# Kernel optimization log

Measured on AMD Instinct MI355X. Metric: run time of the kernel, lower is better.

## Reference

```python
import jax, jax.numpy as jnp
import numpy as np

B, N, E, H = 2, 2048, 768, 12
D = E // H          # head_dim = 64
G = 16              # gate_dim
LN_EPS = 1e-5


def setup_inputs() -> dict:
    key = jax.random.key(0)
    ks = jax.random.split(key, 8)
    s = E ** -0.5
    x = jax.random.normal(ks[0], (B, N, E), jnp.float32)
    # per-head negative decay slopes (ALiBi/TNL-style)
    log_slope = -(2.0 ** (-8.0 * (jnp.arange(H, dtype=jnp.float32) + 1.0) / H))
    Wq = jax.random.normal(ks[1], (E, E), jnp.float32) * s
    Wk = jax.random.normal(ks[2], (E, E), jnp.float32) * s
    Wv = jax.random.normal(ks[3], (E, E), jnp.float32) * s
    Wo = jax.random.normal(ks[4], (E, E), jnp.float32) * s
    Wg1 = jax.random.normal(ks[5], (E, G), jnp.float32) * s
    Wg2 = jax.random.normal(ks[6], (G, E), jnp.float32) * (G ** -0.5)
    ln_w = jnp.ones((E,), jnp.float32)
    ln_b = jnp.zeros((E,), jnp.float32)
    return {"x": x, "log_slope": log_slope, "Wq": Wq, "Wk": Wk, "Wv": Wv,
            "Wo": Wo, "Wg1": Wg1, "Wg2": Wg2, "ln_w": ln_w, "ln_b": ln_b}


def _layernorm(x, w, b):
    mu = jnp.mean(x, axis=-1, keepdims=True)
    var = jnp.mean(jnp.square(x - mu), axis=-1, keepdims=True)
    return (x - mu) * jax.lax.rsqrt(var + LN_EPS) * w + b


def reference(x, log_slope, Wq, Wk, Wv, Wo, Wg1, Wg2, ln_w, ln_b):
    b, n, e = x.shape
    h = log_slope.shape[0]
    d = e // h
    silu = jax.nn.silu
    q = silu(x @ Wq).reshape(b, n, h, d).transpose(0, 2, 1, 3)  # b h n d
    k = silu(x @ Wk).reshape(b, n, h, d).transpose(0, 2, 1, 3)
    v = silu(x @ Wv).reshape(b, n, h, d).transpose(0, 2, 1, 3)

    # exp-decay causal mask: exp(log_slope * (i - j)) for i >= j, else 0
    idx = jnp.arange(n, dtype=jnp.float32)
    diff = idx[:, None] - idx[None, :]                    # n x m
    keep = diff >= 0
    decay = jnp.where(keep,
                      jnp.exp(log_slope[:, None, None] * jnp.maximum(diff, 0.0)),
                      0.0)                                # h n m

    energy = jnp.einsum('bhnd,bhmd->bhnm', q, k) * decay  # b h n m
    out = jnp.einsum('bhnm,bhmd->bhnd', energy, v)        # b h n d
    out = out.transpose(0, 2, 1, 3).reshape(b, n, e)

    gate = jax.nn.sigmoid((x @ Wg1) @ Wg2)                # low-rank output gate
    out = out * gate
    out = out @ Wo
    out = _layernorm(out, ln_w, ln_b)                     # norm_pos='post'
    return out
```

## Files before the change

### kernel.cpp

```cpp
#include <hip/hip_runtime.h>
#include <stdint.h>

#define BB 2
#define NN 2048
#define EE 768
#define HH 12
#define DD 64
#define GG 16

typedef unsigned short u16;
typedef unsigned int u32;
typedef __attribute__((ext_vector_type(8))) short short8;
typedef __attribute__((ext_vector_type(4))) float f32x4;
typedef __attribute__((ext_vector_type(4))) unsigned short u16x4;

__device__ __forceinline__ u16 f2bf(float f) {
  union { float f; u32 u; } a; a.f = f;
  u32 r = a.u + 0x7FFFu + ((a.u >> 16) & 1u);
  return (u16)(r >> 16);
}
__device__ __forceinline__ float bf2f(short s) {
  union { u32 u; float f; } a; a.u = ((u32)(u16)s) << 16; return a.f;
}

__device__ __forceinline__ float silu_f(float v) { return v / (1.f + __expf(-v)); }

__device__ __forceinline__ void gload16(const u16* g, char* l) {
  __builtin_amdgcn_global_load_lds(
      (const __attribute__((address_space(1))) void*)(g),
      (__attribute__((address_space(3))) void*)(l), 16, 0, 0);
}

template<int ROWS>
__device__ __forceinline__ void stage_tile(const u16* __restrict__ gb, int ld, int row0, int col0,
                                           char* lds, int tid) {
  int wid = tid >> 6;
#pragma unroll
  for (int it = 0; it < ROWS / 32; ++it) {
    int c = it * 256 + tid;
    int r = c >> 3;
    int g = (c & 7) ^ (r & 7);
    gload16(gb + (size_t)(row0 + r) * ld + col0 + g * 8,
            lds + (it * 256 + wid * 64) * 16);
  }
}

__device__ __forceinline__ void stage_S(const u16* __restrict__ base, char* lds, int tid, int plane) {
  int wid = tid >> 6;
#pragma unroll
  for (int it = 0; it < 2; ++it) {
    int c = it * 256 + tid;
    int r = c >> 3;
    int g = (c & 7) ^ (r & 7);
    gload16(base + (r >> 4) * 2048 + plane * 1024 + (r & 15) * 64 + g * 8,
            lds + (it * 256 + wid * 64) * 16);
  }
}

__device__ __forceinline__ short8 read_frag(const char* lds, int row, int gk) {
  return *(const short8*)(lds + (((row << 3) | (gk ^ (row & 7))) << 4));
}

__device__ __forceinline__ short8 scale_frag(short8 f, float sc) {
  short8 o;
#pragma unroll
  for (int i = 0; i < 8; ++i) o[i] = (short)f2bf(bf2f(f[i]) * sc);
  return o;
}

__global__ __launch_bounds__(256) void xconv_kernel(const float* __restrict__ x, u16* __restrict__ xb) {
  int i = blockIdx.x * 256 + threadIdx.x;
  float4 v = ((const float4*)x)[i];
  u16x4 o;
  o.x = f2bf(v.x); o.y = f2bf(v.y); o.z = f2bf(v.z); o.w = f2bf(v.w);
  ((u16x4*)xb)[i] = o;
}

__global__ __launch_bounds__(256) void wconv_kernel(const float* __restrict__ Wq, const float* __restrict__ Wk,
    const float* __restrict__ Wv, const float* __restrict__ Wo,
    u16* __restrict__ Wqt, u16* __restrict__ Wkt, u16* __restrict__ Wvt, u16* __restrict__ Wot) {
  const float* src; u16* dst;
  int z = blockIdx.z;
  if (z == 0)      { src = Wq; dst = Wqt; }
  else if (z == 1) { src = Wk; dst = Wkt; }
  else if (z == 2) { src = Wv; dst = Wvt; }
  else             { src = Wo; dst = Wot; }
  __shared__ float tb[64][65];
  int k0 = blockIdx.x * 64, n0 = blockIdx.y * 64;
  int tid = threadIdx.x;
#pragma unroll
  for (int i = 0; i < 16; ++i) {
    int idx = i * 256 + tid;
    int r = idx >> 6, c = idx & 63;
    tb[r][c] = src[(size_t)(k0 + r) * EE + n0 + c];
  }
  __syncthreads();
#pragma unroll
  for (int i = 0; i < 16; ++i) {
    int idx = i * 256 + tid;
    int rn = idx >> 6, ck = idx & 63;
    dst[(size_t)(n0 + rn) * EE + k0 + ck] = f2bf(tb[ck][rn]);
  }
}

__global__ __launch_bounds__(256) void tg_kernel(const float* __restrict__ x, const float* __restrict__ Wg1,
                                                 float* __restrict__ tg) {
  int tid = threadIdx.x, lane = tid & 63, wid = tid >> 6;
  int m = blockIdx.x * 4 + wid;
  int col = lane & 15, sl = lane >> 4;
  const float* xr = x + (size_t)m * EE + sl * 192;
  float acc = 0.f;
#pragma unroll 4
  for (int i = 0; i < 48; ++i) {
    float4 xv = ((const float4*)xr)[i];
    int kk = sl * 192 + i * 4;
    acc += xv.x * Wg1[(kk + 0) * GG + col];
    acc += xv.y * Wg1[(kk + 1) * GG + col];
    acc += xv.z * Wg1[(kk + 2) * GG + col];
    acc += xv.w * Wg1[(kk + 3) * GG + col];
  }
  acc += __shfl_down(acc, 32);
  acc += __shfl_down(acc, 16);
  if (lane < 16) tg[(size_t)m * GG + col] = acc;
}

__global__ __launch_bounds__(256) void qkv_gemm(const u16* __restrict__ xb,
    const u16* __restrict__ Wqt, const u16* __restrict__ Wkt, const u16* __restrict__ Wvt,
    u16* __restrict__ qp, u16* __restrict__ kp, u16* __restrict__ vtp) {
  __shared__ __attribute__((aligned(16))) char As[16384];
  __shared__ __attribute__((aligned(16))) char Zs[16384];
  int tid = threadIdx.x, lane = tid & 63, wid = tid >> 6;
  int m0 = blockIdx.x * 128, n0 = blockIdx.y * 128, w = blockIdx.z;
  const u16* Zt = (w == 0) ? Wqt : (w == 1) ? Wkt : Wvt;
  int wm = wid >> 1, wn = wid & 1;
  f32x4 acc[4][4] = {};
  for (int kt = 0; kt < EE / 64; ++kt) {
    __syncthreads();
    stage_tile<128>(xb, EE, m0, kt * 64, As, tid);
    stage_tile<128>(Zt, EE, n0, kt * 64, Zs, tid);
    __syncthreads();
    short8 af[2][4], bfr[2][4];
#pragma unroll
    for (int ds = 0; ds < 2; ++ds) {
      int gk = ds * 4 + (lane >> 4);
#pragma unroll
      for (int i = 0; i < 4; ++i) {
        af[ds][i]  = read_frag(As, wm * 64 + i * 16 + (lane & 15), gk);
        bfr[ds][i] = read_frag(Zs, wn * 64 + i * 16 + (lane & 15), gk);
      }
    }
#pragma unroll
    for (int mi = 0; mi < 4; ++mi)
#pragma unroll
      for (int ni = 0; ni < 4; ++ni) {
        acc[mi][ni] = __builtin_amdgcn_mfma_f32_16x16x32_bf16(af[0][mi], bfr[0][ni], acc[mi][ni], 0, 0, 0);
        acc[mi][ni] = __builtin_amdgcn_mfma_f32_16x16x32_bf16(af[1][mi], bfr[1][ni], acc[mi][ni], 0, 0, 0);
      }
  }
#pragma unroll
  for (int mi = 0; mi < 4; ++mi) {
    int mbase = m0 + wm * 64 + mi * 16 + ((lane >> 4) << 2);
    int bidx = mbase >> 11, nbase = mbase & 2047;
#pragma unroll
    for (int ni = 0; ni < 4; ++ni) {
      int e = n0 + wn * 64 + ni * 16 + (lane & 15);
      int h = e >> 6, d = e & 63;
      u16 v0 = f2bf(silu_f(acc[mi][ni][0]));
      u16 v1 = f2bf(silu_f(acc[mi][ni][1]));
      u16 v2 = f2bf(silu_f(acc[mi][ni][2]));
      u16 v3 = f2bf(silu_f(acc[mi][ni][3]));
      if (w < 2) {
        u16* dst = (w == 0 ? qp : kp) + (size_t)(bidx * HH + h) * NN * DD + d;
        dst[(size_t)(nbase + 0) * DD] = v0;
        dst[(size_t)(nbase + 1) * DD] = v1;
        dst[(size_t)(nbase + 2) * DD] = v2;
        dst[(size_t)(nbase + 3) * DD] = v3;
      } else {
        u16x4 pk; pk.x = v0; pk.y = v1; pk.z = v2; pk.w = v3;
        *(u16x4*)(vtp + (size_t)((bidx * HH + h) * DD + d) * NN + nbase) = pk;
      }
    }
  }
}

__global__ __launch_bounds__(256) void ktrans_kernel(const u16* __restrict__ kp, u16* __restrict__ ktb) {
  __shared__ u32 tb[64][65];
  int c = blockIdx.x, bh = blockIdx.y, tid = threadIdx.x;
  const u16* src = kp + (size_t)bh * NN * DD + (size_t)c * 64 * DD;
  u16* dst = ktb + (size_t)bh * DD * NN + c * 64;
#pragma unroll
  for (int i = 0; i < 4; ++i) {
    int idx = i * 256 + tid;
    int r = idx >> 4, q = idx & 15;
    u16x4 v = *(const u16x4*)(src + r * 64 + q * 4);
    tb[r][q * 4 + 0] = v.x; tb[r][q * 4 + 1] = v.y;
    tb[r][q * 4 + 2] = v.z; tb[r][q * 4 + 3] = v.w;
  }
  __syncthreads();
#pragma unroll
  for (int i = 0; i < 16; ++i) {
    int idx = i * 256 + tid;
    int d = idx >> 6, n = idx & 63;
    dst[(size_t)d * NN + n] = (u16)tb[n][d];
  }
}

__global__ __launch_bounds__(256) void lstate_kernel(const u16* __restrict__ ktp,
    const u16* __restrict__ vtp, const float* __restrict__ slopes, float* __restrict__ Lst) {
  __shared__ __attribute__((aligned(16))) char KTs[8192];
  __shared__ __attribute__((aligned(16))) char VTs[8192];
  int tid = threadIdx.x, lane = tid & 63, wid = tid >> 6;
  int quad = lane >> 4, l15 = lane & 15;
  int c = blockIdx.x, bh = blockIdx.y, h = bh % HH;
  float slope = slopes[h];
  const u16* ktb = ktp + (size_t)bh * DD * NN;
  const u16* vtb = vtp + (size_t)bh * DD * NN;
  stage_tile<64>(vtb, NN, 0, c * 64, VTs, tid);
  stage_tile<64>(ktb, NN, 0, c * 64, KTs, tid);
  __syncthreads();
  f32x4 acc[4] = {};
  float em = __expf(-slope);
#pragma unroll
  for (int ks = 0; ks < 2; ++ks) {
    int kg = ks * 4 + quad;
    short8 vf = read_frag(VTs, wid * 16 + l15, kg);
    float f = __expf(slope * (float)(64 - kg * 8));
    short8 vdf;
#pragma unroll
    for (int jj = 0; jj < 8; ++jj) { vdf[jj] = (short)f2bf(bf2f(vf[jj]) * f); f *= em; }
#pragma unroll
    for (int dt = 0; dt < 4; ++dt)
      acc[dt] = __builtin_amdgcn_mfma_f32_16x16x32_bf16(
          vdf, read_frag(KTs, dt * 16 + l15, kg), acc[dt], 0, 0, 0);
  }
  float* Lo = Lst + ((size_t)bh * 32 + c) * 4096;
#pragma unroll
  for (int dt = 0; dt < 4; ++dt)
#pragma unroll
    for (int r = 0; r < 4; ++r)
      Lo[(wid * 16 + quad * 4 + r) * 64 + dt * 16 + l15] = acc[dt][r];
}

__global__ __launch_bounds__(256) void scan_kernel(float* __restrict__ Lst,
                                                   const float* __restrict__ slopes) {
  int g = blockIdx.x, bh = blockIdx.y, h = bh % HH, t = threadIdx.x;
  float D = __expf(slopes[h] * 64.f);
  float* base = Lst + (size_t)bh * 32 * 4096;
  int off = g * 1024 + t * 4;
  float4 acc = {0.f, 0.f, 0.f, 0.f};
  float4 nxt = *(float4*)(base + off);
  for (int c = 0; c < 31; ++c) {
    float4 cur = nxt;
    if (c + 1 < 31) nxt = *(float4*)(base + (size_t)(c + 1) * 4096 + off);
    acc.x = acc.x * D + cur.x;
    acc.y = acc.y * D + cur.y;
    acc.z = acc.z * D + cur.z;
    acc.w = acc.w * D + cur.w;
    u16x4 hi, lo;
    float a[4] = {acc.x, acc.y, acc.z, acc.w};
    u16 hv[4], lv[4];
#pragma unroll
    for (int i = 0; i < 4; ++i) {
      hv[i] = f2bf(a[i]);
      lv[i] = f2bf(a[i] - bf2f((short)hv[i]));
    }
    hi.x = hv[0]; hi.y = hv[1]; hi.z = hv[2]; hi.w = hv[3];
    lo.x = lv[0]; lo.y = lv[1]; lo.z = lv[2]; lo.w = lv[3];
    __syncthreads();
    u16* sb = (u16*)(base + (size_t)c * 4096);
    int wo = g * 2048 + (t >> 4) * 64 + (t & 15) * 4;
    *(u16x4*)(sb + wo) = hi;
    *(u16x4*)(sb + wo + 1024) = lo;
  }
}

__global__ __launch_bounds__(256) void attn_chunk(const u16* __restrict__ qp,
    const u16* __restrict__ kp, const u16* __restrict__ vtp,
    const float* __restrict__ slopes, const float* __restrict__ Lst, u16* __restrict__ attnb) {
  __shared__ __attribute__((aligned(16))) char Ks[8192];
  __shared__ __attribute__((aligned(16))) char Vs[8192];
  __shared__ __attribute__((aligned(16))) char Sh[8192];
  __shared__ __attribute__((aligned(16))) char Sl[8192];
  __shared__ __attribute__((aligned(16))) char Ps[4][2304];
  int tid = threadIdx.x, lane = tid & 63, wid = tid >> 6;
  int quad = lane >> 4, l15 = lane & 15;
  int c = blockIdx.x, bh = blockIdx.y, b = bh / HH, h = bh % HH;
  float slope = slopes[h];
  int q0 = c * 64;
  const u16* qbh = qp + (size_t)bh * NN * DD;
  const u16* kbh = kp + (size_t)bh * NN * DD;
  const u16* vbh = vtp + (size_t)bh * DD * NN;

  stage_tile<64>(kbh, DD, q0, 0, Ks, tid);
  stage_tile<64>(vbh, NN, 0, q0, Vs, tid);
  if (c > 0) {
    const u16* sb = (const u16*)(Lst + ((size_t)bh * 32 + (c - 1)) * 4096);
    stage_S(sb, Sh, tid, 0);
    stage_S(sb, Sl, tid, 1);
  }
  int qrow = q0 + wid * 16 + l15;
  short8 qf0 = *(const short8*)(qbh + (size_t)qrow * DD + (quad << 3));
  short8 qf1 = *(const short8*)(qbh + (size_t)qrow * DD + 32 + (quad << 3));
  __syncthreads();

  f32x4 oacc[4] = {};
  char* Pw = Ps[wid];
  int qbase = q0 + wid * 16 + (quad << 2);

  float t_hi = (float)(q0 + 63);
  float rex[4];
#pragma unroll
  for (int r = 0; r < 4; ++r) rex[r] = __expf(slope * ((float)(qbase + r) - t_hi));
#pragma unroll
  for (int jt = 0; jt < 4; ++jt) {
    f32x4 s = {};
    s = __builtin_amdgcn_mfma_f32_16x16x32_bf16(qf0, read_frag(Ks, jt * 16 + l15, quad), s, 0, 0, 0);
    s = __builtin_amdgcn_mfma_f32_16x16x32_bf16(qf1, read_frag(Ks, jt * 16 + l15, 4 + quad), s, 0, 0, 0);
    int jg = q0 + jt * 16 + l15;
    float cex = __expf(slope * (t_hi - (float)jg));
#pragma unroll
    for (int r = 0; r < 4; ++r) {
      int diff = qbase + r - jg;
      float val = (diff >= 0) ? s[r] * rex[r] * cex : 0.f;
      *(u16*)(Pw + (((quad << 2) + r) * 72 + jt * 16 + l15) * 2) = f2bf(val);
    }
  }
  __asm__ volatile("s_waitcnt lgkmcnt(0)" ::: "memory");
#pragma unroll
  for (int ks = 0; ks < 2; ++ks) {
    short8 pf = *(const short8*)(Pw + l15 * 144 + ks * 64 + (quad << 4));
#pragma unroll
    for (int dt = 0; dt < 4; ++dt) {
      oacc[dt] = __builtin_amdgcn_mfma_f32_16x16x32_bf16(
          pf, read_frag(Vs, dt * 16 + l15, ks * 4 + quad), oacc[dt], 0, 0, 0);
    }
  }

  if (c > 0) {
    int il = wid * 16 + l15;
    float qsc = __expf(slope * (float)il);
    short8 qd0 = scale_frag(qf0, qsc);
    short8 qd1 = scale_frag(qf1, qsc);
#pragma unroll
    for (int dt = 0; dt < 4; ++dt) {
      oacc[dt] = __builtin_amdgcn_mfma_f32_16x16x32_bf16(qd0, read_frag(Sh, dt * 16 + l15, quad), oacc[dt], 0, 0, 0);
      oacc[dt] = __builtin_amdgcn_mfma_f32_16x16x32_bf16(qd1, read_frag(Sh, dt * 16 + l15, 4 + quad), oacc[dt], 0, 0, 0);
      oacc[dt] = __builtin_amdgcn_mfma_f32_16x16x32_bf16(qd0, read_frag(Sl, dt * 16 + l15, quad), oacc[dt], 0, 0, 0);
      oacc[dt] = __builtin_amdgcn_mfma_f32_16x16x32_bf16(qd1, read_frag(Sl, dt * 16 + l15, 4 + quad), oacc[dt], 0, 0, 0);
    }
  }

#pragma unroll
  for (int dt = 0; dt < 4; ++dt)
#pragma unroll
    for (int r = 0; r < 4; ++r) {
      int qi = qbase + r;
      int e = h * 64 + dt * 16 + l15;
      attnb[(size_t)(b * NN + qi) * EE + e] = f2bf(oacc[dt][r]);
    }
}

__global__ __launch_bounds__(256) void gate_kernel(u16* __restrict__ attnb, const float* __restrict__ tg,
    const float* __restrict__ Wg2) {
  int m0 = blockIdx.x * 8;
  __shared__ float ts[8][16];
  int tid = threadIdx.x;
  if (tid < 128) ts[tid >> 4][tid & 15] = tg[(size_t)(m0 + (tid >> 4)) * GG + (tid & 15)];
  __syncthreads();
  for (int e = tid; e < EE; e += 256) {
    float wv[16];
#pragma unroll
    for (int g = 0; g < 16; ++g) wv[g] = Wg2[g * EE + e];
#pragma unroll
    for (int r = 0; r < 8; ++r) {
      float gg = 0.f;
#pragma unroll
      for (int g = 0; g < 16; ++g) gg += ts[r][g] * wv[g];
      float sg = 1.f / (1.f + __expf(-gg));
      size_t idx = (size_t)(m0 + r) * EE + e;
      attnb[idx] = f2bf(bf2f((short)attnb[idx]) * sg);
    }
  }
}

__global__ __launch_bounds__(256) void wo_gemm(const u16* __restrict__ A, const u16* __restrict__ Zt,
                                               float* __restrict__ Y) {
  __shared__ __attribute__((aligned(16))) char As[16384];
  __shared__ __attribute__((aligned(16))) char Zs[16384];
  int tid = threadIdx.x, lane = tid & 63, wid = tid >> 6;
  int m0 = blockIdx.x * 128, n0 = blockIdx.y * 128;
  int wm = wid >> 1, wn = wid & 1;
  f32x4 acc[4][4] = {};
  for (int kt = 0; kt < EE / 64; ++kt) {
    __syncthreads();
    stage_tile<128>(A, EE, m0, kt * 64, As, tid);
    stage_tile<128>(Zt, EE, n0, kt * 64, Zs, tid);
    __syncthreads();
    short8 af[2][4], bfr[2][4];
#pragma unroll
    for (int ds = 0; ds < 2; ++ds) {
      int gk = ds * 4 + (lane >> 4);
#pragma unroll
      for (int i = 0; i < 4; ++i) {
        af[ds][i]  = read_frag(As, wm * 64 + i * 16 + (lane & 15), gk);
        bfr[ds][i] = read_frag(Zs, wn * 64 + i * 16 + (lane & 15), gk);
      }
    }
#pragma unroll
    for (int mi = 0; mi < 4; ++mi)
#pragma unroll
      for (int ni = 0; ni < 4; ++ni) {
        acc[mi][ni] = __builtin_amdgcn_mfma_f32_16x16x32_bf16(af[0][mi], bfr[0][ni], acc[mi][ni], 0, 0, 0);
        acc[mi][ni] = __builtin_amdgcn_mfma_f32_16x16x32_bf16(af[1][mi], bfr[1][ni], acc[mi][ni], 0, 0, 0);
      }
  }
#pragma unroll
  for (int mi = 0; mi < 4; ++mi) {
    int mbase = m0 + wm * 64 + mi * 16 + ((lane >> 4) << 2);
#pragma unroll
    for (int ni = 0; ni < 4; ++ni) {
      int e = n0 + wn * 64 + ni * 16 + (lane & 15);
#pragma unroll
      for (int r = 0; r < 4; ++r)
        Y[(size_t)(mbase + r) * EE + e] = acc[mi][ni][r];
    }
  }
}

__global__ __launch_bounds__(256) void ln_kernel(const float* __restrict__ y, const float* __restrict__ w,
    const float* __restrict__ bb, float* __restrict__ out) {
  int m = blockIdx.x, tid = threadIdx.x;
  const float* yr = y + (size_t)m * EE;
  float v0 = yr[tid], v1 = yr[tid + 256], v2 = yr[tid + 512];
  float s = v0 + v1 + v2;
  float s2 = v0 * v0 + v1 * v1 + v2 * v2;
#pragma unroll
  for (int off = 32; off > 0; off >>= 1) {
    s += __shfl_down(s, off);
    s2 += __shfl_down(s2, off);
  }
  __shared__ float ss[4], ssq[4];
  int lane = tid & 63, wid = tid >> 6;
  if (lane == 0) { ss[wid] = s; ssq[wid] = s2; }
  __syncthreads();
  s = ss[0] + ss[1] + ss[2] + ss[3];
  s2 = ssq[0] + ssq[1] + ssq[2] + ssq[3];
  float mu = s * (1.f / 768.f);
  float var = s2 * (1.f / 768.f) - mu * mu;
  float rs = rsqrtf(var + 1e-5f);
  float* orow = out + (size_t)m * EE;
  orow[tid]       = (v0 - mu) * rs * w[tid]       + bb[tid];
  orow[tid + 256] = (v1 - mu) * rs * w[tid + 256] + bb[tid + 256];
  orow[tid + 512] = (v2 - mu) * rs * w[tid + 512] + bb[tid + 512];
}

extern "C" void kernel_launch(void* const* d_in, const int* in_sizes, int n_in,
                              void* d_out, int out_size, void* d_ws, size_t ws_size,
                              hipStream_t stream) {
  (void)in_sizes; (void)n_in; (void)out_size; (void)ws_size;
  const float* x   = (const float*)d_in[0];
  const float* ls  = (const float*)d_in[1];
  const float* Wq  = (const float*)d_in[2];
  const float* Wk  = (const float*)d_in[3];
  const float* Wv  = (const float*)d_in[4];
  const float* Wo  = (const float*)d_in[5];
  const float* Wg1 = (const float*)d_in[6];
  const float* Wg2 = (const float*)d_in[7];
  const float* lnw = (const float*)d_in[8];
  const float* lnb = (const float*)d_in[9];

  char* p = (char*)d_ws;
  u16* xb    = (u16*)(p + 0);
  u16* kt2   = (u16*)(p + 0);
  u16* attnb = (u16*)(p + 0);
  u16* Wqt   = (u16*)(p + 6291456);
  u16* Wkt   = (u16*)(p + 7471104);
  u16* Wvt   = (u16*)(p + 8650752);
  u16* Wot   = (u16*)(p + 9830400);
  u16* qq    = (u16*)(p + 11010048);
  u16* kk    = (u16*)(p + 17301504);
  u16* vt    = (u16*)(p + 23592960);
  float* tg  = (float*)(p + 29884416);
  float* Lst = (float*)(p + 30146560);
  float* yy  = (float*)(p + 11010048);
  float* out = (float*)d_out;

  hipLaunchKernelGGL(xconv_kernel, dim3(3072), dim3(256), 0, stream, x, xb);
  hipLaunchKernelGGL(wconv_kernel, dim3(12, 12, 4), dim3(256), 0, stream, Wq, Wk, Wv, Wo, Wqt, Wkt, Wvt, Wot);
  hipLaunchKernelGGL(tg_kernel, dim3(1024), dim3(256), 0, stream, x, Wg1, tg);
  hipLaunchKernelGGL(qkv_gemm, dim3(32, 6, 3), dim3(256), 0, stream, xb, Wqt, Wkt, Wvt, qq, kk, vt);
  hipLaunchKernelGGL(ktrans_kernel, dim3(32, 24), dim3(256), 0, stream, kk, kt2);
  hipLaunchKernelGGL(lstate_kernel, dim3(32, 24), dim3(256), 0, stream, kt2, vt, ls, Lst);
  hipLaunchKernelGGL(scan_kernel, dim3(4, 24), dim3(256), 0, stream, Lst, ls);
  hipLaunchKernelGGL(attn_chunk, dim3(32, 24), dim3(256), 0, stream, qq, kk, vt, ls, Lst, attnb);
  hipLaunchKernelGGL(gate_kernel, dim3(512), dim3(256), 0, stream, attnb, tg, Wg2);
  hipLaunchKernelGGL(wo_gemm, dim3(32, 6), dim3(256), 0, stream, attnb, Wot, yy);
  hipLaunchKernelGGL(ln_kernel, dim3(4096), dim3(256), 0, stream, yy, lnw, lnb, out);
}
```

Measured before the change: 187.7 us.

## Fuse K transpose into QKV GEMM, gate into attention, halve GEMM M-tiles

```diff
diff --git a/kernel.cpp b/kernel.cpp
--- a/kernel.cpp
+++ b/kernel.cpp
@@ -126,31 +126,33 @@
 
 __global__ __launch_bounds__(256) void qkv_gemm(const u16* __restrict__ xb,
     const u16* __restrict__ Wqt, const u16* __restrict__ Wkt, const u16* __restrict__ Wvt,
-    u16* __restrict__ qp, u16* __restrict__ kp, u16* __restrict__ vtp) {
-  __shared__ __attribute__((aligned(16))) char As[16384];
+    u16* __restrict__ qp, u16* __restrict__ kp, u16* __restrict__ ktp, u16* __restrict__ vtp) {
+  __shared__ __attribute__((aligned(16))) char As[8192];
   __shared__ __attribute__((aligned(16))) char Zs[16384];
   int tid = threadIdx.x, lane = tid & 63, wid = tid >> 6;
-  int m0 = blockIdx.x * 128, n0 = blockIdx.y * 128, w = blockIdx.z;
+  int quad = lane >> 4, l15 = lane & 15;
+  int m0 = blockIdx.x * 64, n0 = blockIdx.y * 128, w = blockIdx.z;
   const u16* Zt = (w == 0) ? Wqt : (w == 1) ? Wkt : Wvt;
   int wm = wid >> 1, wn = wid & 1;
-  f32x4 acc[4][4] = {};
+  f32x4 acc[2][4] = {};
   for (int kt = 0; kt < EE / 64; ++kt) {
     __syncthreads();
-    stage_tile<128>(xb, EE, m0, kt * 64, As, tid);
+    stage_tile<64>(xb, EE, m0, kt * 64, As, tid);
     stage_tile<128>(Zt, EE, n0, kt * 64, Zs, tid);
     __syncthreads();
-    short8 af[2][4], bfr[2][4];
+    short8 af[2][2], bfr[2][4];
 #pragma unroll
     for (int ds = 0; ds < 2; ++ds) {
-      int gk = ds * 4 + (lane >> 4);
-#pragma unroll
-      for (int i = 0; i < 4; ++i) {
-        af[ds][i]  = read_frag(As, wm * 64 + i * 16 + (lane & 15), gk);
-        bfr[ds][i] = read_frag(Zs, wn * 64 + i * 16 + (lane & 15), gk);
-      }
-    }
-#pragma unroll
-    for (int mi = 0; mi < 4; ++mi)
+      int gk = ds * 4 + quad;
+#pragma unroll
+      for (int i = 0; i < 2; ++i)
+        af[ds][i] = read_frag(As, wm * 32 + i * 16 + l15, gk);
+#pragma unroll
+      for (int i = 0; i < 4; ++i)
+        bfr[ds][i] = read_frag(Zs, wn * 64 + i * 16 + l15, gk);
+    }
+#pragma unroll
+    for (int mi = 0; mi < 2; ++mi)
 #pragma unroll
       for (int ni = 0; ni < 4; ++ni) {
         acc[mi][ni] = __builtin_amdgcn_mfma_f32_16x16x32_bf16(af[0][mi], bfr[0][ni], acc[mi][ni], 0, 0, 0);
@@ -158,12 +160,12 @@
       }
   }
 #pragma unroll
-  for (int mi = 0; mi < 4; ++mi) {
-    int mbase = m0 + wm * 64 + mi * 16 + ((lane >> 4) << 2);
+  for (int mi = 0; mi < 2; ++mi) {
+    int mbase = m0 + wm * 32 + mi * 16 + (quad << 2);
     int bidx = mbase >> 11, nbase = mbase & 2047;
 #pragma unroll
     for (int ni = 0; ni < 4; ++ni) {
-      int e = n0 + wn * 64 + ni * 16 + (lane & 15);
+      int e = n0 + wn * 64 + ni * 16 + l15;
       int h = e >> 6, d = e & 63;
       u16 v0 = f2bf(silu_f(acc[mi][ni][0]));
       u16 v1 = f2bf(silu_f(acc[mi][ni][1]));
@@ -175,33 +177,15 @@
         dst[(size_t)(nbase + 1) * DD] = v1;
         dst[(size_t)(nbase + 2) * DD] = v2;
         dst[(size_t)(nbase + 3) * DD] = v3;
+        if (w == 1) {
+          u16x4 pk; pk.x = v0; pk.y = v1; pk.z = v2; pk.w = v3;
+          *(u16x4*)(ktp + (size_t)((bidx * HH + h) * DD + d) * NN + nbase) = pk;
+        }
       } else {
         u16x4 pk; pk.x = v0; pk.y = v1; pk.z = v2; pk.w = v3;
         *(u16x4*)(vtp + (size_t)((bidx * HH + h) * DD + d) * NN + nbase) = pk;
       }
     }
-  }
-}
-
-__global__ __launch_bounds__(256) void ktrans_kernel(const u16* __restrict__ kp, u16* __restrict__ ktb) {
-  __shared__ u32 tb[64][65];
-  int c = blockIdx.x, bh = blockIdx.y, tid = threadIdx.x;
-  const u16* src = kp + (size_t)bh * NN * DD + (size_t)c * 64 * DD;
-  u16* dst = ktb + (size_t)bh * DD * NN + c * 64;
-#pragma unroll
-  for (int i = 0; i < 4; ++i) {
-    int idx = i * 256 + tid;
-    int r = idx >> 4, q = idx & 15;
-    u16x4 v = *(const u16x4*)(src + r * 64 + q * 4);
-    tb[r][q * 4 + 0] = v.x; tb[r][q * 4 + 1] = v.y;
-    tb[r][q * 4 + 2] = v.z; tb[r][q * 4 + 3] = v.w;
-  }
-  __syncthreads();
-#pragma unroll
-  for (int i = 0; i < 16; ++i) {
-    int idx = i * 256 + tid;
-    int d = idx >> 6, n = idx & 63;
-    dst[(size_t)d * NN + n] = (u16)tb[n][d];
   }
 }
 
@@ -276,12 +260,15 @@
 
 __global__ __launch_bounds__(256) void attn_chunk(const u16* __restrict__ qp,
     const u16* __restrict__ kp, const u16* __restrict__ vtp,
-    const float* __restrict__ slopes, const float* __restrict__ Lst, u16* __restrict__ attnb) {
+    const float* __restrict__ slopes, const float* __restrict__ Lst,
+    const float* __restrict__ tgp, const float* __restrict__ Wg2, u16* __restrict__ attnb) {
   __shared__ __attribute__((aligned(16))) char Ks[8192];
   __shared__ __attribute__((aligned(16))) char Vs[8192];
   __shared__ __attribute__((aligned(16))) char Sh[8192];
   __shared__ __attribute__((aligned(16))) char Sl[8192];
   __shared__ __attribute__((aligned(16))) char Ps[4][2304];
+  __shared__ float ts[64][16];
+  __shared__ float w2[16][64];
   int tid = threadIdx.x, lane = tid & 63, wid = tid >> 6;
   int quad = lane >> 4, l15 = lane & 15;
   int c = blockIdx.x, bh = blockIdx.y, b = bh / HH, h = bh % HH;
@@ -298,6 +285,12 @@
     stage_S(sb, Sh, tid, 0);
     stage_S(sb, Sl, tid, 1);
   }
+  {
+    float4 tv = *(const float4*)(tgp + ((size_t)(b * NN + q0) + (tid >> 2)) * GG + (tid & 3) * 4);
+    *(float4*)&ts[tid >> 2][(tid & 3) * 4] = tv;
+    float4 wv = *(const float4*)(Wg2 + (size_t)(tid >> 4) * EE + h * 64 + (tid & 15) * 4);
+    *(float4*)&w2[tid >> 4][(tid & 15) * 4] = wv;
+  }
   int qrow = q0 + wid * 16 + l15;
   short8 qf0 = *(const short8*)(qbh + (size_t)qrow * DD + (quad << 3));
   short8 qf1 = *(const short8*)(qbh + (size_t)qrow * DD + 32 + (quad << 3));
@@ -351,6 +344,21 @@
   }
 
 #pragma unroll
+  for (int r = 0; r < 4; ++r) {
+    int row = wid * 16 + (quad << 2) + r;
+    float gv[4] = {0.f, 0.f, 0.f, 0.f};
+#pragma unroll
+    for (int g = 0; g < 16; ++g) {
+      float tv = ts[row][g];
+#pragma unroll
+      for (int dt = 0; dt < 4; ++dt) gv[dt] += tv * w2[g][dt * 16 + l15];
+    }
+#pragma unroll
+    for (int dt = 0; dt < 4; ++dt)
+      oacc[dt][r] *= 1.f / (1.f + __expf(-gv[dt]));
+  }
+
+#pragma unroll
   for (int dt = 0; dt < 4; ++dt)
 #pragma unroll
     for (int r = 0; r < 4; ++r) {
@@ -360,54 +368,33 @@
     }
 }
 
-__global__ __launch_bounds__(256) void gate_kernel(u16* __restrict__ attnb, const float* __restrict__ tg,
-    const float* __restrict__ Wg2) {
-  int m0 = blockIdx.x * 8;
-  __shared__ float ts[8][16];
-  int tid = threadIdx.x;
-  if (tid < 128) ts[tid >> 4][tid & 15] = tg[(size_t)(m0 + (tid >> 4)) * GG + (tid & 15)];
-  __syncthreads();
-  for (int e = tid; e < EE; e += 256) {
-    float wv[16];
-#pragma unroll
-    for (int g = 0; g < 16; ++g) wv[g] = Wg2[g * EE + e];
-#pragma unroll
-    for (int r = 0; r < 8; ++r) {
-      float gg = 0.f;
-#pragma unroll
-      for (int g = 0; g < 16; ++g) gg += ts[r][g] * wv[g];
-      float sg = 1.f / (1.f + __expf(-gg));
-      size_t idx = (size_t)(m0 + r) * EE + e;
-      attnb[idx] = f2bf(bf2f((short)attnb[idx]) * sg);
-    }
-  }
-}
-
 __global__ __launch_bounds__(256) void wo_gemm(const u16* __restrict__ A, const u16* __restrict__ Zt,
                                                float* __restrict__ Y) {
-  __shared__ __attribute__((aligned(16))) char As[16384];
+  __shared__ __attribute__((aligned(16))) char As[8192];
   __shared__ __attribute__((aligned(16))) char Zs[16384];
   int tid = threadIdx.x, lane = tid & 63, wid = tid >> 6;
-  int m0 = blockIdx.x * 128, n0 = blockIdx.y * 128;
+  int quad = lane >> 4, l15 = lane & 15;
+  int m0 = blockIdx.x * 64, n0 = blockIdx.y * 128;
   int wm = wid >> 1, wn = wid & 1;
-  f32x4 acc[4][4] = {};
+  f32x4 acc[2][4] = {};
   for (int kt = 0; kt < EE / 64; ++kt) {
     __syncthreads();
-    stage_tile<128>(A, EE, m0, kt * 64, As, tid);
+    stage_tile<64>(A, EE, m0, kt * 64, As, tid);
     stage_tile<128>(Zt, EE, n0, kt * 64, Zs, tid);
     __syncthreads();
-    short8 af[2][4], bfr[2][4];
+    short8 af[2][2], bfr[2][4];
 #pragma unroll
     for (int ds = 0; ds < 2; ++ds) {
-      int gk = ds * 4 + (lane >> 4);
-#pragma unroll
-      for (int i = 0; i < 4; ++i) {
-        af[ds][i]  = read_frag(As, wm * 64 + i * 16 + (lane & 15), gk);
-        bfr[ds][i] = read_frag(Zs, wn * 64 + i * 16 + (lane & 15), gk);
-      }
-    }
-#pragma unroll
-    for (int mi = 0; mi < 4; ++mi)
+      int gk = ds * 4 + quad;
+#pragma unroll
+      for (int i = 0; i < 2; ++i)
+        af[ds][i] = read_frag(As, wm * 32 + i * 16 + l15, gk);
+#pragma unroll
+      for (int i = 0; i < 4; ++i)
+        bfr[ds][i] = read_frag(Zs, wn * 64 + i * 16 + l15, gk);
+    }
+#pragma unroll
+    for (int mi = 0; mi < 2; ++mi)
 #pragma unroll
       for (int ni = 0; ni < 4; ++ni) {
         acc[mi][ni] = __builtin_amdgcn_mfma_f32_16x16x32_bf16(af[0][mi], bfr[0][ni], acc[mi][ni], 0, 0, 0);
@@ -415,11 +402,11 @@
       }
   }
 #pragma unroll
-  for (int mi = 0; mi < 4; ++mi) {
-    int mbase = m0 + wm * 64 + mi * 16 + ((lane >> 4) << 2);
+  for (int mi = 0; mi < 2; ++mi) {
+    int mbase = m0 + wm * 32 + mi * 16 + (quad << 2);
 #pragma unroll
     for (int ni = 0; ni < 4; ++ni) {
-      int e = n0 + wn * 64 + ni * 16 + (lane & 15);
+      int e = n0 + wn * 64 + ni * 16 + l15;
 #pragma unroll
       for (int r = 0; r < 4; ++r)
         Y[(size_t)(mbase + r) * EE + e] = acc[mi][ni][r];
@@ -471,7 +458,6 @@
 
   char* p = (char*)d_ws;
   u16* xb    = (u16*)(p + 0);
-  u16* kt2   = (u16*)(p + 0);
   u16* attnb = (u16*)(p + 0);
   u16* Wqt   = (u16*)(p + 6291456);
   u16* Wkt   = (u16*)(p + 7471104);
@@ -482,18 +468,17 @@
   u16* vt    = (u16*)(p + 23592960);
   float* tg  = (float*)(p + 29884416);
   float* Lst = (float*)(p + 30146560);
+  u16* kt2   = (u16*)(p + 42729472);
   float* yy  = (float*)(p + 11010048);
   float* out = (float*)d_out;
 
   hipLaunchKernelGGL(xconv_kernel, dim3(3072), dim3(256), 0, stream, x, xb);
   hipLaunchKernelGGL(wconv_kernel, dim3(12, 12, 4), dim3(256), 0, stream, Wq, Wk, Wv, Wo, Wqt, Wkt, Wvt, Wot);
   hipLaunchKernelGGL(tg_kernel, dim3(1024), dim3(256), 0, stream, x, Wg1, tg);
-  hipLaunchKernelGGL(qkv_gemm, dim3(32, 6, 3), dim3(256), 0, stream, xb, Wqt, Wkt, Wvt, qq, kk, vt);
-  hipLaunchKernelGGL(ktrans_kernel, dim3(32, 24), dim3(256), 0, stream, kk, kt2);
+  hipLaunchKernelGGL(qkv_gemm, dim3(64, 6, 3), dim3(256), 0, stream, xb, Wqt, Wkt, Wvt, qq, kk, kt2, vt);
   hipLaunchKernelGGL(lstate_kernel, dim3(32, 24), dim3(256), 0, stream, kt2, vt, ls, Lst);
   hipLaunchKernelGGL(scan_kernel, dim3(4, 24), dim3(256), 0, stream, Lst, ls);
-  hipLaunchKernelGGL(attn_chunk, dim3(32, 24), dim3(256), 0, stream, qq, kk, vt, ls, Lst, attnb);
-  hipLaunchKernelGGL(gate_kernel, dim3(512), dim3(256), 0, stream, attnb, tg, Wg2);
-  hipLaunchKernelGGL(wo_gemm, dim3(32, 6), dim3(256), 0, stream, attnb, Wot, yy);
+  hipLaunchKernelGGL(attn_chunk, dim3(32, 24), dim3(256), 0, stream, qq, kk, vt, ls, Lst, tg, Wg2, attnb);
+  hipLaunchKernelGGL(wo_gemm, dim3(64, 6), dim3(256), 0, stream, attnb, Wot, yy);
   hipLaunchKernelGGL(ln_kernel, dim3(4096), dim3(256), 0, stream, yy, lnw, lnb, out);
 }
```

After: 171.3 us. 1.1x faster.
